# Performance work log

Hardware: AMD Instinct MI355X
Metric: run time of the kernel (lower is better)

## Reference

```python
import jax, jax.numpy as jnp
import numpy as np

B, C, H, W = 32, 384, 32, 32
NH = 4            # num_heads
CC = 192          # conv_channels = ceil(384/2)
HID = 1536        # mlp hidden = 4*dim
EPS = 1e-6


def _ln2d(x, w, b):
    # LayerNorm over channel axis of NCHW
    u = x.mean(1, keepdims=True)
    s = ((x - u) ** 2).mean(1, keepdims=True)
    return w[:, None, None] * ((x - u) * jax.lax.rsqrt(s + EPS)) + b[:, None, None]


def setup_inputs() -> dict:
    key = jax.random.key(0)
    ks = jax.random.split(key, 8)
    f = lambda k, shp, sc: jax.random.normal(k, shp, jnp.float32) * sc
    return {
        "x": f(ks[0], (B, C, H, W), 1.0),
        "conv_w": f(ks[1], (CC, 1, 3, 3), 0.1),
        "conv_b": jnp.zeros((CC,), jnp.float32),
        "nxca_w": jnp.ones((C,), jnp.float32),
        "nxca_b": jnp.zeros((C,), jnp.float32),
        "temp": jnp.ones((NH, 1, 1), jnp.float32),
        "qkv_w": f(ks[2], (3 * C, C), 0.05),
        "qkv_b": jnp.zeros((3 * C,), jnp.float32),
        "proj_w": f(ks[3], (C, C), 0.05),
        "proj_b": jnp.zeros((C,), jnp.float32),
        "norm_w": jnp.ones((C,), jnp.float32),
        "norm_b": jnp.zeros((C,), jnp.float32),
        "fc1_w": f(ks[4], (HID, C), 0.05),
        "fc1_b": jnp.zeros((HID,), jnp.float32),
        "fc2_w": f(ks[5], (C, HID), 0.05),
        "fc2_b": jnp.zeros((C,), jnp.float32),
        "gamma_xca": jnp.ones((C,), jnp.float32),
        "gamma": jnp.ones((C,), jnp.float32),
    }


def reference(x, conv_w, conv_b, nxca_w, nxca_b, temp, qkv_w, qkv_b,
              proj_w, proj_b, norm_w, norm_b, fc1_w, fc1_b, fc2_w, fc2_b,
              gamma_xca, gamma):
    b, c, h, w = x.shape
    n = h * w
    hd = c // NH
    # depthwise 3x3 conv on first CC channels (in-place in torch -> shortcut
    # taken AFTER the conv, faithfully reproduced here)
    xc = jax.lax.conv_general_dilated(
        x[:, :CC], conv_w, (1, 1), ((1, 1), (1, 1)), feature_group_count=CC
    ) + conv_b[None, :, None, None]
    x = jnp.concatenate([xc, x[:, CC:]], axis=1)
    shortcut = x
    # XCA branch
    y = _ln2d(x, nxca_w, nxca_b)
    yf = y.reshape(b, c, n).transpose(0, 2, 1)                       # [B,N,C]
    qkv = (yf @ qkv_w.T + qkv_b).reshape(b, n, 3, NH, hd).transpose(2, 0, 3, 1, 4)
    q, k, v = qkv[0], qkv[1], qkv[2]                                  # [B,h,N,hd]
    q = q / jnp.maximum(jnp.linalg.norm(q, axis=-1, keepdims=True), 1e-12)
    k = k / jnp.maximum(jnp.linalg.norm(k, axis=-1, keepdims=True), 1e-12)
    attn = jax.nn.softmax(jnp.einsum('bhnd,bhmd->bhnm', q, k) * temp, axis=-1)
    o = jnp.einsum('bhnm,bhmd->bhnd', attn, v).transpose(0, 2, 1, 3).reshape(b, n, c)
    o = (o @ proj_w.T + proj_b).transpose(0, 2, 1).reshape(b, c, h, w)
    x = shortcut + gamma_xca[None, :, None, None] * o
    # MLP branch
    shortcut2 = x
    z = _ln2d(x, norm_w, norm_b).transpose(0, 2, 3, 1).reshape(b, n, c)
    z = jax.nn.gelu(z @ fc1_w.T + fc1_b, approximate=False) @ fc2_w.T + fc2_b
    z = z.reshape(b, h, w, c).transpose(0, 3, 1, 2)
    return shortcut2 + gamma[None, :, None, None] * z
```

## Files before the change

kernel.cpp:

```cpp
#include <hip/hip_runtime.h>
#include <cstdint>

typedef unsigned short u16;
typedef unsigned int u32;
typedef unsigned long long u64;
typedef __attribute__((ext_vector_type(4))) float f32x4;
typedef __attribute__((ext_vector_type(16))) float f32x16;
typedef __attribute__((ext_vector_type(8))) __bf16 bf16x8;
typedef __attribute__((ext_vector_type(8))) u16 u16x8;
typedef __attribute__((ext_vector_type(4))) u32 u32x4;
typedef __attribute__((ext_vector_type(2))) int i32x2;

#define DEV __device__ __forceinline__

DEV u16 cvt16(float f) {
  __bf16 h = (__bf16)f;
  return __builtin_bit_cast(u16, h);
}
DEV u16 f2bf(float f) {
  u32 u = __builtin_bit_cast(u32, f);
  u += 0x7fffu + ((u >> 16) & 1u);
  return (u16)(u >> 16);
}
DEV float bflo2f(u32 packed) { return __builtin_bit_cast(float, packed << 16); }
DEV float bfhi2f(u32 packed) { return __builtin_bit_cast(float, packed & 0xffff0000u); }

DEV void g2l16(void* lds_wave_base, const void* gsrc) {
  __builtin_amdgcn_global_load_lds(
      (const __attribute__((address_space(1))) u32*)gsrc,
      (__attribute__((address_space(3))) u32*)lds_wave_base, 16, 0, 0);
}

DEV float gelu_tanh(float v) {
  float z = v * (0.7978845608f + 0.0356774081f * v * v);
  float e = __expf(2.0f * z);
  float th = 1.0f - 2.0f / (e + 1.0f);
  return 0.5f * v * (1.0f + th);
}

__global__ __launch_bounds__(256) void conv_k(const float* __restrict__ x,
                                              const float* __restrict__ cw,
                                              const float* __restrict__ cb,
                                              float* __restrict__ xc) {
  const int bc = blockIdx.x;
  const int c = bc % 384;
  const int p4 = threadIdx.x * 4;
  const float* xp = x + ((size_t)bc << 10);
  float* op = xc + ((size_t)bc << 10) + p4;
  if (c >= 192) {
    *(f32x4*)op = *(const f32x4*)(xp + p4);
    return;
  }
  const int hh = p4 >> 5, ww0 = p4 & 31;
  const float* wb = cw + c * 9;
  float b0 = cb[c];
  float a0 = b0, a1 = b0, a2 = b0, a3 = b0;
#pragma unroll
  for (int dy = 0; dy < 3; ++dy) {
    int y = hh + dy - 1;
    if ((unsigned)y < 32u) {
      const float* rp = xp + y * 32 + ww0;
      f32x4 m = *(const f32x4*)rp;
      float lft = (ww0 > 0) ? rp[-1] : 0.f;
      float rgt = (ww0 < 28) ? rp[4] : 0.f;
      float w0 = wb[dy * 3], w1 = wb[dy * 3 + 1], w2 = wb[dy * 3 + 2];
      a0 += lft * w0 + m[0] * w1 + m[1] * w2;
      a1 += m[0] * w0 + m[1] * w1 + m[2] * w2;
      a2 += m[1] * w0 + m[2] * w1 + m[3] * w2;
      a3 += m[2] * w0 + m[3] * w1 + rgt * w2;
    }
  }
  f32x4 r = {a0, a1, a2, a3};
  *(f32x4*)op = r;
}

__global__ __launch_bounds__(256) void cvt4_k(const float* __restrict__ s0,
                                              const float* __restrict__ s1,
                                              const float* __restrict__ s2,
                                              const float* __restrict__ s3,
                                              u16* __restrict__ d0,
                                              u16* __restrict__ d1,
                                              u16* __restrict__ d2,
                                              u16* __restrict__ d3) {
  int id = blockIdx.x * 256 + threadIdx.x;
  if (id < 442368) d0[id] = f2bf(s0[id]);
  else if (id < 589824) d1[id - 442368] = f2bf(s1[id - 442368]);
  else if (id < 1179648) d2[id - 589824] = f2bf(s2[id - 589824]);
  else if (id < 1769472) d3[id - 1179648] = f2bf(s3[id - 1179648]);
}

__global__ __launch_bounds__(256) void ln_t_k(const float* __restrict__ X,
                                              const float* __restrict__ w,
                                              const float* __restrict__ bsh,
                                              u16* __restrict__ Y) {
  __shared__ float tile[384][33];
  __shared__ float ps[8][32], ps2[8][32];
  __shared__ float mean_s[32], rstd_s[32];
  const int b = blockIdx.y;
  const int p0 = blockIdx.x * 32;
  const int t = threadIdx.x;
  const int pl = t & 31, cg = t >> 5;
  const float* xb = X + (((size_t)b * 384) << 10) + p0 + pl;
  float s = 0.f, s2 = 0.f;
  for (int c = cg; c < 384; c += 8) {
    float v = xb[(size_t)c << 10];
    tile[c][pl] = v;
    s += v;
    s2 += v * v;
  }
  ps[cg][pl] = s;
  ps2[cg][pl] = s2;
  __syncthreads();
  if (t < 32) {
    float a = 0.f, a2 = 0.f;
#pragma unroll
    for (int g = 0; g < 8; ++g) { a += ps[g][t]; a2 += ps2[g][t]; }
    float mu = a * (1.f / 384.f);
    float var = a2 * (1.f / 384.f) - mu * mu;
    mean_s[t] = mu;
    rstd_s[t] = rsqrtf(var + 1e-6f);
  }
  __syncthreads();
  const int cl = t & 63, pg = t >> 6;
  for (int p = pg; p < 32; p += 4) {
    float mu = mean_s[p], rs = rstd_s[p];
    size_t orow = (((size_t)b << 10) + p0 + p) * 384;
#pragma unroll
    for (int cc = 0; cc < 6; ++cc) {
      int c = cc * 64 + cl;
      float v = (tile[c][p] - mu) * rs * w[c] + bsh[c];
      Y[orow + c] = f2bf(v);
    }
  }
}

__global__ __launch_bounds__(256) void normk_k(u16* __restrict__ QKV) {
  const int t = threadIdx.x;
  const int w = t >> 6, l = t & 63;
  const int rg = l >> 4, li = l & 15;
  const int tok = blockIdx.x * 16 + w * 4 + rg;
  u16* rowp = QKV + (size_t)tok * 1152 + 384;
#pragma unroll
  for (int h = 0; h < 4; ++h) {
    u16* p = rowp + h * 96 + li * 6;
    u32 a = *(const u32*)p;
    u32 b2 = *(const u32*)(p + 2);
    u32 c = *(const u32*)(p + 4);
    float v[6] = {bflo2f(a), bfhi2f(a), bflo2f(b2), bfhi2f(b2), bflo2f(c), bfhi2f(c)};
    float ss = 0.f;
#pragma unroll
    for (int i = 0; i < 6; ++i) ss += v[i] * v[i];
#pragma unroll
    for (int mk = 1; mk < 16; mk <<= 1) ss += __shfl_xor(ss, mk, 64);
    float sc = 1.0f / fmaxf(sqrtf(ss), 1e-12f);
    u32 o0 = (u32)f2bf(v[0] * sc) | ((u32)f2bf(v[1] * sc) << 16);
    u32 o1 = (u32)f2bf(v[2] * sc) | ((u32)f2bf(v[3] * sc) << 16);
    u32 o2 = (u32)f2bf(v[4] * sc) | ((u32)f2bf(v[5] * sc) << 16);
    *(u32*)p = o0;
    *(u32*)(p + 2) = o1;
    *(u32*)(p + 4) = o2;
  }
}

__global__ __launch_bounds__(256, 3) void attn_k(const u16* __restrict__ QKV,
                                                 const u16* __restrict__ Vg,
                                                 u16* __restrict__ O,
                                                 const float* __restrict__ temp) {
  __shared__ u16 Kt[2][6656];
  __shared__ u16 Vt[2][6144];
  const int t = threadIdx.x;
  const int w = t >> 6, l = t & 63;
  const int l31 = l & 31, hi = l >> 5;
  const int id = blockIdx.x;
  const int xcd = id & 7, jj = id >> 3;
  const int bh = xcd * 16 + (jj >> 3);
  const int qb = jj & 7;
  const int b = bh >> 2, h = bh & 3;
  const int q0 = qb * 128 + w * 32;
  const u16* Qb = QKV + (size_t)b * 1024 * 1152;
  const char* Kbg = (const char*)QKV + (size_t)b * 1024 * 2304 + 768 + 192 * h;
  const char* Vbg = (const char*)(Vg + (size_t)bh * 98304);
  const float tl2e = temp[h] * 1.44269504f;
  const float mT2 = -fabsf(temp[h]) * 1.44269504f;

  u32 kOff[4], vOff[3];
#pragma unroll
  for (int i = 0; i < 4; ++i) {
    int s = (i < 3) ? (i * 256 + t) : (768 + w * 16 + (l & 15));
    int row = s / 13, c = s - row * 13;
    kOff[i] = row * 2304 + ((c < 12) ? c * 16 : 0);
  }
#pragma unroll
  for (int i = 0; i < 3; ++i) {
    int s = i * 256 + t;
    int row = s >> 3, cb = (s & 7) * 16;
    vOff[i] = row * 2048 + (cb ^ ((row & 7) << 4));
  }

  bf16x8 qf[6];
  {
    const u16* qp = Qb + (size_t)(q0 + l31) * 1152 + h * 96 + hi * 8;
#pragma unroll
    for (int kc = 0; kc < 6; ++kc) qf[kc] = *(const bf16x8*)(qp + kc * 16);
  }
  float alpha;
  {
    float ss = 0.f;
#pragma unroll
    for (int kc = 0; kc < 6; ++kc)
#pragma unroll
      for (int e = 0; e < 8; ++e) {
        float v = (float)qf[kc][e];
        ss += v * v;
      }
    ss += __shfl_xor(ss, 32, 64);
    alpha = tl2e * rsqrtf(fmaxf(ss, 1e-24f));
  }

  f32x16 oa[3];
#pragma unroll
  for (int dt = 0; dt < 3; ++dt)
#pragma unroll
    for (int r = 0; r < 16; ++r) oa[dt][r] = 0.f;
  float l_r = 0.f;

#define STAGE(buf, kv0)                                                        \
  {                                                                            \
    const char* kb = Kbg + (size_t)(kv0) * 2304;                               \
    const char* vb = Vbg + (size_t)(kv0) * 2;                                  \
    char* kd = (char*)&Kt[buf][0];                                             \
    char* vd = (char*)&Vt[buf][0];                                             \
    g2l16(kd + w * 1024, kb + kOff[0]);                                        \
    g2l16(kd + 4096 + w * 1024, kb + kOff[1]);                                 \
    g2l16(kd + 8192 + w * 1024, kb + kOff[2]);                                 \
    if (l < 16) g2l16(kd + 12288 + w * 256, kb + kOff[3]);                     \
    g2l16(vd + w * 1024, vb + vOff[0]);                                        \
    g2l16(vd + 4096 + w * 1024, vb + vOff[1]);                                 \
    g2l16(vd + 8192 + w * 1024, vb + vOff[2]);                                 \
  }

  STAGE(0, 0);
  for (int tt = 0; tt < 16; ++tt) {
    const int cur = tt & 1;
    if (tt < 15) {
      STAGE(cur ^ 1, (tt + 1) * 64);
      asm volatile("s_waitcnt vmcnt(7)" ::: "memory");
    } else {
      asm volatile("s_waitcnt vmcnt(0)" ::: "memory");
    }
    __builtin_amdgcn_s_barrier();
    const char* Kc = (const char*)&Kt[cur][0];
    const char* Vc = (const char*)&Vt[cur][0];
    f32x16 st[2];
#pragma unroll
    for (int n = 0; n < 2; ++n)
#pragma unroll
      for (int r = 0; r < 16; ++r) st[n][r] = 0.f;
#pragma unroll
    for (int n = 0; n < 2; ++n) {
      const char* krow = Kc + (n * 32 + l31) * 208 + hi * 16;
#pragma unroll
      for (int kc = 0; kc < 6; ++kc) {
        bf16x8 kf = *(const bf16x8*)(krow + kc * 32);
        st[n] = __builtin_amdgcn_mfma_f32_32x32x16_bf16(kf, qf[kc], st[n], 0, 0, 0);
      }
    }
    u32 pk[2][8];
#pragma unroll
    for (int n = 0; n < 2; ++n) {
      float p[16];
#pragma unroll
      for (int r = 0; r < 16; ++r) {
        p[r] = exp2f(fmaf(st[n][r], alpha, mT2));
        l_r += p[r];
      }
#pragma unroll
      for (int m = 0; m < 8; ++m)
        pk[n][m] = (u32)cvt16(p[2 * m]) | ((u32)cvt16(p[2 * m + 1]) << 16);
    }
#pragma unroll
    for (int c = 0; c < 4; ++c) {
      const int n = c >> 1, cc = c & 1;
      i32x2 s1 = __builtin_amdgcn_permlane32_swap((int)pk[n][4 * cc],
                                                  (int)pk[n][4 * cc + 2], 0, 0);
      i32x2 s2 = __builtin_amdgcn_permlane32_swap((int)pk[n][4 * cc + 1],
                                                  (int)pk[n][4 * cc + 3], 0, 0);
      u32x4 wd;
      wd[0] = (u32)s1[0]; wd[1] = (u32)s2[0];
      wd[2] = (u32)s1[1]; wd[3] = (u32)s2[1];
      bf16x8 pa = __builtin_bit_cast(bf16x8, wd);
      const u32 vcol = (u32)((c * 32 + hi * 16) ^ ((l31 & 7) << 4));
#pragma unroll
      for (int dt = 0; dt < 3; ++dt) {
        bf16x8 vf = *(const bf16x8*)(Vc + (dt * 32 + l31) * 128 + vcol);
        oa[dt] = __builtin_amdgcn_mfma_f32_32x32x16_bf16(pa, vf, oa[dt], 0, 0, 0);
      }
    }
    __builtin_amdgcn_s_barrier();
  }
#undef STAGE
  l_r += __shfl_xor(l_r, 32, 64);
  float inv = 1.0f / l_r;
#pragma unroll
  for (int r = 0; r < 16; ++r) {
    const int qr = (r & 3) + 8 * (r >> 2) + 4 * hi;
    float invr = __shfl(inv, qr, 64);
    const int tok = q0 + qr;
    u16* orow = O + ((size_t)b * 1024 + tok) * 384 + h * 96;
#pragma unroll
    for (int dt = 0; dt < 3; ++dt)
      orow[dt * 32 + l31] = f2bf(oa[dt][r] * invr);
  }
}

template <int EPI>
__global__ __launch_bounds__(512) void gemm256_k(const u16* __restrict__ A,
                                                 const u16* __restrict__ B,
                                                 int N, int K,
                                                 const float* __restrict__ bias,
                                                 u16* __restrict__ vtp,
                                                 u16* __restrict__ outp,
                                                 int nbx) {
  __shared__ u16 SM[24576];
  const int t = threadIdx.x;
  const int w = t >> 6, l = t & 63;
  const int l15 = l & 15, kg = l >> 4;
  const int id = blockIdx.x;
  const int xcd = id & 7, jj = id >> 3;
  const int qq = jj / nbx;
  const int bx = jj - qq * nbx;
  const int by = xcd * 16 + qq;
  const int m0 = by * 256, n0 = bx * 128;
  const int wr = w >> 1, wc = w & 1;
  const size_t ldab = (size_t)K * 2;
  const char* pa1 = (const char*)A + (size_t)(m0 + (t >> 2)) * ldab + (t & 3) * 16;
  const char* pa2 = pa1 + (size_t)128 * ldab;
  const char* pb1 = (const char*)B + (size_t)(n0 + (t >> 2)) * ldab + (t & 3) * 16;
  char* SMc = (char*)SM;

  f32x4 acc[4][4];
#pragma unroll
  for (int m = 0; m < 4; ++m)
#pragma unroll
    for (int n = 0; n < 4; ++n) acc[m][n] = {0.f, 0.f, 0.f, 0.f};

  const int nkt = K >> 5;
  g2l16(SMc + w * 1024, pa1);
  g2l16(SMc + 8192 + w * 1024, pa2);
  g2l16(SMc + 32768 + w * 1024, pb1);
  for (int kt = 0; kt < nkt; ++kt) {
    const int buf = kt & 1;
    if (kt + 1 < nkt) {
      const size_t o = (size_t)(kt + 1) * 64;
      g2l16(SMc + (buf ^ 1) * 16384 + w * 1024, pa1 + o);
      g2l16(SMc + (buf ^ 1) * 16384 + 8192 + w * 1024, pa2 + o);
      g2l16(SMc + 32768 + (buf ^ 1) * 8192 + w * 1024, pb1 + o);
      asm volatile("s_waitcnt vmcnt(3)" ::: "memory");
    } else {
      asm volatile("s_waitcnt vmcnt(0)" ::: "memory");
    }
    __builtin_amdgcn_s_barrier();
    __builtin_amdgcn_sched_barrier(0);
    const u16* Ab = SM + buf * 8192;
    const u16* Bb = SM + 16384 + buf * 4096;
    bf16x8 af[4], bfr[4];
#pragma unroll
    for (int m = 0; m < 4; ++m)
      af[m] = *(const bf16x8*)(Ab + (wr * 64 + m * 16 + l15) * 32 + kg * 8);
#pragma unroll
    for (int n = 0; n < 4; ++n)
      bfr[n] = *(const bf16x8*)(Bb + (wc * 64 + n * 16 + l15) * 32 + kg * 8);
    __builtin_amdgcn_s_setprio(1);
#pragma unroll
    for (int m = 0; m < 4; ++m)
#pragma unroll
      for (int n = 0; n < 4; ++n)
        acc[m][n] = __builtin_amdgcn_mfma_f32_16x16x32_bf16(af[m], bfr[n], acc[m][n], 0, 0, 0);
    __builtin_amdgcn_s_setprio(0);
    __builtin_amdgcn_sched_barrier(0);
    __builtin_amdgcn_s_barrier();
  }

  if (EPI == 4 && n0 >= 768) {
#pragma unroll
    for (int m = 0; m < 4; ++m) {
      const int tokbase = m0 + wr * 64 + m * 16 + kg * 4;
      const int bb = tokbase >> 10, nb = tokbase & 1023;
#pragma unroll
      for (int n = 0; n < 4; ++n) {
        int within = n0 - 768 + wc * 64 + n * 16 + l15;
        int hh = within / 96;
        int dd = within - hh * 96;
        float bs = bias[768 + within];
        int bh = bb * 4 + hh;
        u64 pk = 0;
#pragma unroll
        for (int j = 0; j < 4; ++j)
          pk |= (u64)cvt16(acc[m][n][j] + bs) << (16 * j);
        *(u64*)(vtp + ((size_t)bh * 96 + dd) * 1024 + nb) = pk;
      }
    }
    return;
  }

  u16* Ct = SM;
  float bs[4];
#pragma unroll
  for (int n = 0; n < 4; ++n) bs[n] = bias[n0 + wc * 64 + n * 16 + l15];
  const size_t ostride = (EPI == 4) ? 1152 : (size_t)N;
#pragma unroll
  for (int p = 0; p < 2; ++p) {
    if ((wr >> 1) == p) {
      u16* cw_ = Ct + ((wr & 1) * 64 + kg * 4) * 128 + wc * 64 + l15;
#pragma unroll
      for (int m = 0; m < 4; ++m)
#pragma unroll
        for (int n = 0; n < 4; ++n)
#pragma unroll
          for (int j = 0; j < 4; ++j) {
            float v = acc[m][n][j] + bs[n];
            if (EPI == 1) v = gelu_tanh(v);
            cw_[(m * 16 + j) * 128 + n * 16] = cvt16(v);
          }
    }
    __syncthreads();
    const int row_l = t >> 2;
    const int colc = (t & 3) * 32;
    const u16* src = Ct + row_l * 128 + colc;
    u16* dst = outp + (size_t)(m0 + p * 128 + row_l) * ostride + n0 + colc;
#pragma unroll
    for (int c4 = 0; c4 < 4; ++c4)
      *(u16x8*)(dst + c4 * 8) = *(const u16x8*)(src + c4 * 8);
    __syncthreads();
  }
}

__global__ __launch_bounds__(256) void gemm_k(const u16* __restrict__ A,
                                              const u16* __restrict__ B,
                                              int K,
                                              const float* __restrict__ bias,
                                              const float* __restrict__ gamma,
                                              const float* __restrict__ res,
                                              float* __restrict__ outp) {
  __shared__ u16 SM[16384];
  const int t = threadIdx.x;
  const int w = t >> 6, l = t & 63;
  const int l15 = l & 15, kg = l >> 4;
  int id = blockIdx.x;
  int xcd = id & 7, jj = id >> 3;
  int by = jj % 3;
  int bx = (jj / 3) * 8 + xcd;
  const int m0 = by * 128, n0 = bx * 128;
  const int wr = w >> 1, wc = w & 1;

  const size_t ldab = (size_t)K * 2;
  const char* pa1 = (const char*)A + (size_t)(m0 + (t >> 2)) * ldab + (t & 3) * 16;
  const char* pa2 = pa1 + (size_t)64 * ldab;
  const char* pb1 = (const char*)B + (size_t)(n0 + (t >> 2)) * ldab + (t & 3) * 16;
  const char* pb2 = pb1 + (size_t)64 * ldab;
  char* SMc = (char*)SM;

  f32x4 acc[4][4];
#pragma unroll
  for (int m = 0; m < 4; ++m)
#pragma unroll
    for (int n = 0; n < 4; ++n) acc[m][n] = {0.f, 0.f, 0.f, 0.f};

  const int nkt = K >> 5;
  {
    char* ad = SMc + w * 1024;
    char* bd = SMc + 16384 + w * 1024;
    g2l16(ad, pa1); g2l16(ad + 4096, pa2);
    g2l16(bd, pb1); g2l16(bd + 4096, pb2);
  }
  for (int kt = 0; kt < nkt; ++kt) {
    const int buf = kt & 1;
    if (kt + 1 < nkt) {
      const size_t o = (size_t)(kt + 1) * 64;
      char* ad = SMc + (buf ^ 1) * 8192 + w * 1024;
      char* bd = SMc + 16384 + (buf ^ 1) * 8192 + w * 1024;
      g2l16(ad, pa1 + o); g2l16(ad + 4096, pa2 + o);
      g2l16(bd, pb1 + o); g2l16(bd + 4096, pb2 + o);
      asm volatile("s_waitcnt vmcnt(4)" ::: "memory");
    } else {
      asm volatile("s_waitcnt vmcnt(0)" ::: "memory");
    }
    __builtin_amdgcn_s_barrier();
    __builtin_amdgcn_sched_barrier(0);
    const u16* Ab = SM + buf * 4096;
    const u16* Bb = SM + 8192 + buf * 4096;
    bf16x8 af[4], bfr[4];
#pragma unroll
    for (int m = 0; m < 4; ++m)
      af[m] = *(const bf16x8*)(Ab + (wr * 64 + m * 16 + l15) * 32 + kg * 8);
#pragma unroll
    for (int n = 0; n < 4; ++n)
      bfr[n] = *(const bf16x8*)(Bb + (wc * 64 + n * 16 + l15) * 32 + kg * 8);
    __builtin_amdgcn_s_setprio(1);
#pragma unroll
    for (int m = 0; m < 4; ++m)
#pragma unroll
      for (int n = 0; n < 4; ++n)
        acc[m][n] = __builtin_amdgcn_mfma_f32_16x16x32_bf16(af[m], bfr[n], acc[m][n], 0, 0, 0);
    __builtin_amdgcn_s_setprio(0);
    __builtin_amdgcn_sched_barrier(0);
    __builtin_amdgcn_s_barrier();
  }

#pragma unroll
  for (int m = 0; m < 4; ++m) {
#pragma unroll
    for (int n = 0; n < 4; ++n) {
      int tok = n0 + wc * 64 + n * 16 + l15;
      int bb = tok >> 10, p = tok & 1023;
#pragma unroll
      for (int j = 0; j < 4; ++j) {
        int c = m0 + wr * 64 + m * 16 + kg * 4 + j;
        size_t addr = (((size_t)(bb * 384 + c)) << 10) + p;
        outp[addr] = res[addr] + gamma[c] * (acc[m][n][j] + bias[c]);
      }
    }
  }
}

extern "C" void kernel_launch(void* const* d_in, const int* in_sizes, int n_in,
                              void* d_out, int out_size, void* d_ws,
                              size_t ws_size, hipStream_t stream) {
  const float* x      = (const float*)d_in[0];
  const float* conv_w = (const float*)d_in[1];
  const float* conv_b = (const float*)d_in[2];
  const float* nxca_w = (const float*)d_in[3];
  const float* nxca_b = (const float*)d_in[4];
  const float* temp   = (const float*)d_in[5];
  const float* qkv_w  = (const float*)d_in[6];
  const float* qkv_b  = (const float*)d_in[7];
  const float* proj_w = (const float*)d_in[8];
  const float* proj_b = (const float*)d_in[9];
  const float* norm_w = (const float*)d_in[10];
  const float* norm_b = (const float*)d_in[11];
  const float* fc1_w  = (const float*)d_in[12];
  const float* fc1_b  = (const float*)d_in[13];
  const float* fc2_w  = (const float*)d_in[14];
  const float* fc2_b  = (const float*)d_in[15];
  const float* g_xca  = (const float*)d_in[16];
  const float* g_mlp  = (const float*)d_in[17];
  (void)in_sizes; (void)n_in; (void)out_size; (void)ws_size;

  char* ws = (char*)d_ws;
  float* xc  = (float*)(ws);
  u16* Y     = (u16*)(ws + 50331648);
  u16* QKVr  = (u16*)(ws + 75497472);
  u16* Vt    = (u16*)(ws + 150994944);
  u16* Obuf  = Y;
  u16* H1    = QKVr;
  u16* wq    = (u16*)(ws + 176160768);
  u16* wp    = (u16*)(ws + 177045504);
  u16* w1    = (u16*)(ws + 177340416);
  u16* w2    = (u16*)(ws + 178520064);

  cvt4_k<<<6912, 256, 0, stream>>>(qkv_w, proj_w, fc1_w, fc2_w, wq, wp, w1, w2);

  conv_k<<<12288, 256, 0, stream>>>(x, conv_w, conv_b, xc);
  ln_t_k<<<dim3(32, 32), 256, 0, stream>>>(xc, nxca_w, nxca_b, Y);
  gemm256_k<4><<<1152, 512, 0, stream>>>(Y, wq, 1152, 384, qkv_b, Vt, QKVr, 9);
  normk_k<<<2048, 256, 0, stream>>>(QKVr);
  attn_k<<<1024, 256, 0, stream>>>(QKVr, Vt, Obuf, temp);
  gemm_k<<<768, 256, 0, stream>>>(wp, Obuf, 384, proj_b, g_xca, xc, xc);
  ln_t_k<<<dim3(32, 32), 256, 0, stream>>>(xc, norm_w, norm_b, Y);
  gemm256_k<1><<<1536, 512, 0, stream>>>(Y, w1, 1536, 384, fc1_b, nullptr, H1, 12);
  gemm_k<<<768, 256, 0, stream>>>(w2, H1, 1536, fc2_b, g_mlp, xc, (float*)d_out);
}
```

Measured before the change: 396.1 us.

## Restructure GEMM double-buffer sync to one barrier per k-step; vectorize weight cast

Both GEMM kernels now issue the next tile's global-to-LDS loads at the top of each iteration. They then wait for all loads and hit a single barrier after the MFMAs, replacing the earlier wait-then-barrier at the top plus a second barrier at the end. This removes one barrier per k-step, at the cost of an explicit wait on all outstanding loads (vmcnt(0)) after compute. The weight-conversion kernel now processes four floats per thread with vector loads and stores, and launches a quarter as many blocks.

```diff
diff --git a/kernel.cpp b/kernel.cpp
--- a/kernel.cpp
+++ b/kernel.cpp
@@ -8,6 +8,7 @@
 typedef __attribute__((ext_vector_type(16))) float f32x16;
 typedef __attribute__((ext_vector_type(8))) __bf16 bf16x8;
 typedef __attribute__((ext_vector_type(8))) u16 u16x8;
+typedef __attribute__((ext_vector_type(4))) u16 u16x4;
 typedef __attribute__((ext_vector_type(4))) u32 u32x4;
 typedef __attribute__((ext_vector_type(2))) int i32x2;
 
@@ -82,11 +83,18 @@
                                               u16* __restrict__ d1,
                                               u16* __restrict__ d2,
                                               u16* __restrict__ d3) {
-  int id = blockIdx.x * 256 + threadIdx.x;
-  if (id < 442368) d0[id] = f2bf(s0[id]);
-  else if (id < 589824) d1[id - 442368] = f2bf(s1[id - 442368]);
-  else if (id < 1179648) d2[id - 589824] = f2bf(s2[id - 589824]);
-  else if (id < 1769472) d3[id - 1179648] = f2bf(s3[id - 1179648]);
+  int id = (blockIdx.x * 256 + threadIdx.x) * 4;
+  const float* s; u16* d; int off;
+  if (id < 442368) { s = s0; d = d0; off = 0; }
+  else if (id < 589824) { s = s1; d = d1; off = 442368; }
+  else if (id < 1179648) { s = s2; d = d2; off = 589824; }
+  else { s = s3; d = d3; off = 1179648; }
+  int i = id - off;
+  f32x4 v = *(const f32x4*)(s + i);
+  u16x4 o;
+#pragma unroll
+  for (int j = 0; j < 4; ++j) o[j] = f2bf(v[j]);
+  *(u16x4*)(d + i) = o;
 }
 
 __global__ __launch_bounds__(256) void ln_t_k(const float* __restrict__ X,
@@ -344,23 +352,21 @@
 #pragma unroll
     for (int n = 0; n < 4; ++n) acc[m][n] = {0.f, 0.f, 0.f, 0.f};
 
+#define GSTG(bf, kti)                                                          \
+  {                                                                            \
+    const size_t o = (size_t)(kti) * 64;                                       \
+    g2l16(SMc + (bf) * 16384 + w * 1024, pa1 + o);                             \
+    g2l16(SMc + (bf) * 16384 + 8192 + w * 1024, pa2 + o);                      \
+    g2l16(SMc + 32768 + (bf) * 8192 + w * 1024, pb1 + o);                      \
+  }
+
   const int nkt = K >> 5;
-  g2l16(SMc + w * 1024, pa1);
-  g2l16(SMc + 8192 + w * 1024, pa2);
-  g2l16(SMc + 32768 + w * 1024, pb1);
+  GSTG(0, 0);
+  asm volatile("s_waitcnt vmcnt(0)" ::: "memory");
+  __builtin_amdgcn_s_barrier();
   for (int kt = 0; kt < nkt; ++kt) {
     const int buf = kt & 1;
-    if (kt + 1 < nkt) {
-      const size_t o = (size_t)(kt + 1) * 64;
-      g2l16(SMc + (buf ^ 1) * 16384 + w * 1024, pa1 + o);
-      g2l16(SMc + (buf ^ 1) * 16384 + 8192 + w * 1024, pa2 + o);
-      g2l16(SMc + 32768 + (buf ^ 1) * 8192 + w * 1024, pb1 + o);
-      asm volatile("s_waitcnt vmcnt(3)" ::: "memory");
-    } else {
-      asm volatile("s_waitcnt vmcnt(0)" ::: "memory");
-    }
-    __builtin_amdgcn_s_barrier();
-    __builtin_amdgcn_sched_barrier(0);
+    if (kt + 1 < nkt) GSTG(buf ^ 1, kt + 1);
     const u16* Ab = SM + buf * 8192;
     const u16* Bb = SM + 16384 + buf * 4096;
     bf16x8 af[4], bfr[4];
@@ -377,9 +383,11 @@
       for (int n = 0; n < 4; ++n)
         acc[m][n] = __builtin_amdgcn_mfma_f32_16x16x32_bf16(af[m], bfr[n], acc[m][n], 0, 0, 0);
     __builtin_amdgcn_s_setprio(0);
+    asm volatile("s_waitcnt vmcnt(0)" ::: "memory");
+    __builtin_amdgcn_s_barrier();
     __builtin_amdgcn_sched_barrier(0);
-    __builtin_amdgcn_s_barrier();
-  }
+  }
+#undef GSTG
 
   if (EPI == 4 && n0 >= 768) {
 #pragma unroll
@@ -466,27 +474,22 @@
 #pragma unroll
     for (int n = 0; n < 4; ++n) acc[m][n] = {0.f, 0.f, 0.f, 0.f};
 
+#define KSTG(bf, kti)                                                          \
+  {                                                                            \
+    const size_t o = (size_t)(kti) * 64;                                       \
+    char* ad = SMc + (bf) * 8192 + w * 1024;                                   \
+    char* bd = SMc + 16384 + (bf) * 8192 + w * 1024;                           \
+    g2l16(ad, pa1 + o); g2l16(ad + 4096, pa2 + o);                             \
+    g2l16(bd, pb1 + o); g2l16(bd + 4096, pb2 + o);                             \
+  }
+
   const int nkt = K >> 5;
-  {
-    char* ad = SMc + w * 1024;
-    char* bd = SMc + 16384 + w * 1024;
-    g2l16(ad, pa1); g2l16(ad + 4096, pa2);
-    g2l16(bd, pb1); g2l16(bd + 4096, pb2);
-  }
+  KSTG(0, 0);
+  asm volatile("s_waitcnt vmcnt(0)" ::: "memory");
+  __builtin_amdgcn_s_barrier();
   for (int kt = 0; kt < nkt; ++kt) {
     const int buf = kt & 1;
-    if (kt + 1 < nkt) {
-      const size_t o = (size_t)(kt + 1) * 64;
-      char* ad = SMc + (buf ^ 1) * 8192 + w * 1024;
-      char* bd = SMc + 16384 + (buf ^ 1) * 8192 + w * 1024;
-      g2l16(ad, pa1 + o); g2l16(ad + 4096, pa2 + o);
-      g2l16(bd, pb1 + o); g2l16(bd + 4096, pb2 + o);
-      asm volatile("s_waitcnt vmcnt(4)" ::: "memory");
-    } else {
-      asm volatile("s_waitcnt vmcnt(0)" ::: "memory");
-    }
-    __builtin_amdgcn_s_barrier();
-    __builtin_amdgcn_sched_barrier(0);
+    if (kt + 1 < nkt) KSTG(buf ^ 1, kt + 1);
     const u16* Ab = SM + buf * 4096;
     const u16* Bb = SM + 8192 + buf * 4096;
     bf16x8 af[4], bfr[4];
@@ -503,9 +506,11 @@
       for (int n = 0; n < 4; ++n)
         acc[m][n] = __builtin_amdgcn_mfma_f32_16x16x32_bf16(af[m], bfr[n], acc[m][n], 0, 0, 0);
     __builtin_amdgcn_s_setprio(0);
+    asm volatile("s_waitcnt vmcnt(0)" ::: "memory");
+    __builtin_amdgcn_s_barrier();
     __builtin_amdgcn_sched_barrier(0);
-    __builtin_amdgcn_s_barrier();
-  }
+  }
+#undef KSTG
 
 #pragma unroll
   for (int m = 0; m < 4; ++m) {
@@ -558,7 +563,7 @@
   u16* w1    = (u16*)(ws + 177340416);
   u16* w2    = (u16*)(ws + 178520064);
 
-  cvt4_k<<<6912, 256, 0, stream>>>(qkv_w, proj_w, fc1_w, fc2_w, wq, wp, w1, w2);
+  cvt4_k<<<1728, 256, 0, stream>>>(qkv_w, proj_w, fc1_w, fc2_w, wq, wp, w1, w2);
 
   conv_k<<<12288, 256, 0, stream>>>(x, conv_w, conv_b, xc);
   ln_t_k<<<dim3(32, 32), 256, 0, stream>>>(xc, nxca_w, nxca_b, Y);
```

Result: slower. 406.0 us (+2.5%).
